# Performance work log

Measured on AMD Instinct MI355X. Metric: run time of the kernel, lower is better.

The kernel has to match this reference:

```python
import jax, jax.numpy as jnp
import numpy as np

EMBED = 1024
HEADS = 16
HEAD_DIM = EMBED // HEADS


def setup_inputs() -> dict:
    key = jax.random.key(0)
    ks = jax.random.split(key, 5)
    s = 0.02
    x = jax.random.normal(ks[0], (2, 2048, EMBED), dtype=jnp.float32)
    W_qkv = jax.random.normal(ks[1], (EMBED, 3 * EMBED), dtype=jnp.float32) * s
    b_qkv = jnp.zeros((3 * EMBED,), dtype=jnp.float32)
    W_proj = jax.random.normal(ks[2], (EMBED, EMBED), dtype=jnp.float32) * s
    b_proj = jnp.zeros((EMBED,), dtype=jnp.float32)
    return {"x": x, "W_qkv": W_qkv, "b_qkv": b_qkv, "W_proj": W_proj, "b_proj": b_proj}


def reference(x, W_qkv, b_qkv, W_proj, b_proj):
    B, N, _ = x.shape
    scale = HEAD_DIM ** -0.5
    qkv = x @ W_qkv + b_qkv                     # [B,N,3E]
    qkv = qkv.reshape(B, N, 3, HEADS, HEAD_DIM)
    q = qkv[:, :, 0].transpose(0, 2, 1, 3) * scale  # [B,H,N,D]
    k = qkv[:, :, 1].transpose(0, 2, 1, 3)
    v = qkv[:, :, 2].transpose(0, 2, 1, 3)
    attn = jnp.einsum('bhnd,bhmd->bhnm', q, k)  # [B,H,N,N]
    attn = jax.nn.softmax(attn, axis=-1)
    out = jnp.einsum('bhnm,bhmd->bhnd', attn, v)  # [B,H,N,D]
    out = out.transpose(0, 2, 1, 3).reshape(B, N, HEADS * HEAD_DIM)
    return out @ W_proj + b_proj
```

## Files before the change

### kernel.cpp

```cpp
#include <hip/hip_runtime.h>
#include <hip/hip_bf16.h>
#include <stdint.h>

typedef unsigned short u16;
typedef __bf16 bf16x8 __attribute__((ext_vector_type(8)));
typedef float f32x4 __attribute__((ext_vector_type(4)));

__device__ __forceinline__ u16 f2bf(float f) {
    union { float f; unsigned u; } x; x.f = f;
    unsigned u = x.u;
    u += 0x7FFFu + ((u >> 16) & 1u);
    return (u16)(u >> 16);
}

typedef __attribute__((address_space(1))) void gvoid;
typedef __attribute__((address_space(3))) void lvoid;
__device__ __forceinline__ void gl2lds16(const void* g, void* l) {
    __builtin_amdgcn_global_load_lds((gvoid*)g, (lvoid*)l, 16, 0, 0);
}

__global__ __launch_bounds__(256) void prep_kernel(
    const float* __restrict__ x, u16* __restrict__ xb,
    const float* __restrict__ Wqkv, u16* __restrict__ wqkvT,
    const float* __restrict__ Wproj, u16* __restrict__ wprojT)
{
    __shared__ u16 tile[64][65];
    const int blk = blockIdx.x;
    const int tid = threadIdx.x;

    if (blk < 2048) {
        const size_t i = ((size_t)blk * 256 + tid) * 8;
        float4 a = *(const float4*)(x + i);
        float4 b = *(const float4*)(x + i + 4);
        ushort4 oa, ob;
        oa.x = f2bf(a.x); oa.y = f2bf(a.y); oa.z = f2bf(a.z); oa.w = f2bf(a.w);
        ob.x = f2bf(b.x); ob.y = f2bf(b.y); ob.z = f2bf(b.z); ob.w = f2bf(b.w);
        *(ushort4*)(xb + i) = oa;
        *(ushort4*)(xb + i + 4) = ob;
        return;
    }
    const float* in; u16* out; int rows, cols, bx, by;
    if (blk < 2816) { int t = blk - 2048; in = Wqkv;  out = wqkvT;  rows = 1024; cols = 3072; bx = t % 48; by = t / 48; }
    else            { int t = blk - 2816; in = Wproj; out = wprojT; rows = 1024; cols = 1024; bx = t % 16; by = t / 16; }
#pragma unroll
    for (int i = 0; i < 16; i++) {
        int e = i * 256 + tid;
        int r = e >> 6, c = e & 63;
        tile[r][c] = f2bf(in[(size_t)(by * 64 + r) * cols + bx * 64 + c]);
    }
    __syncthreads();
#pragma unroll
    for (int i = 0; i < 16; i++) {
        int e = i * 256 + tid;
        int r = e >> 6, c = e & 63;
        out[(size_t)(bx * 64 + r) * rows + by * 64 + c] = tile[c][r];
    }
}

__global__ __launch_bounds__(256) void transpose_v(
    const u16* __restrict__ in, u16* __restrict__ out)
{
    __shared__ u16 tile[64][65];
    const int bh = blockIdx.y;
    const int t0 = blockIdx.x * 64;
    const u16* ip = in + ((size_t)bh * 2048 + t0) * 64;
    u16* op = out + (size_t)bh * 64 * 2048 + t0;
    const int tid = threadIdx.x;
#pragma unroll
    for (int i = 0; i < 16; i++) {
        int e = i * 256 + tid;
        int r = e >> 6, c = e & 63;
        tile[r][c] = ip[(size_t)r * 64 + c];
    }
    __syncthreads();
#pragma unroll
    for (int i = 0; i < 16; i++) {
        int e = i * 256 + tid;
        int d = e >> 6, tt = e & 63;
        op[(size_t)d * 2048 + tt] = tile[tt][d];
    }
}

__global__ __launch_bounds__(256) void gemm_qkv(
    const u16* __restrict__ A, const u16* __restrict__ Bt,
    const float* __restrict__ bias,
    u16* __restrict__ q, u16* __restrict__ ko, u16* __restrict__ vo)
{
    constexpr int K = 1024;
    __shared__ __align__(16) u16 sA[128 * 64];
    __shared__ __align__(16) u16 sB[128 * 64];
    const int tid = threadIdx.x;
    const int wave = tid >> 6, lane = tid & 63;
    const int quad = lane >> 4, l16 = lane & 15;
    const int wm = (wave >> 1) * 64, wn = (wave & 1) * 64;
    const int m0 = blockIdx.y * 128, n0 = blockIdx.x * 128;
    const int srow = lane >> 3;
    const int scol = (lane & 7) * 8;

    f32x4 acc[4][4];
#pragma unroll
    for (int i = 0; i < 4; i++)
#pragma unroll
        for (int j = 0; j < 4; j++)
#pragma unroll
            for (int r = 0; r < 4; r++) acc[i][j][r] = 0.f;

    for (int kt = 0; kt < K; kt += 64) {
        __syncthreads();
#pragma unroll
        for (int t = 0; t < 4; t++) {
            int rb = wave * 32 + t * 8;
            gl2lds16(A  + (size_t)(m0 + rb + srow) * K + kt + scol, &sA[rb * 64]);
            gl2lds16(Bt + (size_t)(n0 + rb + srow) * K + kt + scol, &sB[rb * 64]);
        }
        __syncthreads();
#pragma unroll
        for (int kk = 0; kk < 64; kk += 32) {
            bf16x8 af[4], bfr[4];
#pragma unroll
            for (int t = 0; t < 4; t++) {
                af[t]  = *(const bf16x8*)&sA[(wm + t * 16 + l16) * 64 + kk + quad * 8];
                bfr[t] = *(const bf16x8*)&sB[(wn + t * 16 + l16) * 64 + kk + quad * 8];
            }
#pragma unroll
            for (int i = 0; i < 4; i++)
#pragma unroll
                for (int j = 0; j < 4; j++)
                    acc[i][j] = __builtin_amdgcn_mfma_f32_16x16x32_bf16(
                        af[i], bfr[j], acc[i][j], 0, 0, 0);
        }
    }

    const float QSCALE = 0.18033688011112042f;
#pragma unroll
    for (int i = 0; i < 4; i++) {
#pragma unroll
        for (int j = 0; j < 4; j++) {
            int n = n0 + wn + j * 16 + l16;
            float bv = bias[n];
            int which = n >> 10, rem = n & 1023;
            int h = rem >> 6, d = rem & 63;
#pragma unroll
            for (int r = 0; r < 4; r++) {
                int m = m0 + wm + i * 16 + quad * 4 + r;
                float v = acc[i][j][r] + bv;
                int b = m >> 11, t = m & 2047;
                size_t idx = ((size_t)(b * 16 + h) * 2048 + t) * 64 + d;
                if (which == 0)
                    q[idx] = f2bf(v * QSCALE);
                else if (which == 1)
                    ko[idx] = f2bf(v);
                else
                    vo[idx] = f2bf(v);
            }
        }
    }
}

__global__ __launch_bounds__(256) void attn_kernel(
    const u16* __restrict__ q, const u16* __restrict__ ko,
    const u16* __restrict__ vt, u16* __restrict__ o)
{
    __shared__ __align__(16) u16 sQ[128 * 72];
    __shared__ __align__(16) u16 sK[64 * 72];
    __shared__ __align__(16) u16 sV[80 * 72];
    __shared__ __align__(16) float sPf[128 * 68];

    const int tid = threadIdx.x;
    const int wave = tid >> 6, lane = tid & 63;
    const int quad = lane >> 4, l16 = lane & 15;

    const int lid = blockIdx.x;
    const int xcd = lid & 7, idx = lid >> 3;
    const int h = xcd * 2 + (idx & 1);
    const int b = (idx >> 1) & 1;
    const int q0 = (idx >> 2) * 128;
    const size_t bh = (size_t)(b * 16 + h);

    const u16* qp  = q  + bh * 2048 * 64;
    const u16* kp  = ko + bh * 2048 * 64;
    const u16* vtp = vt + bh * 64 * 2048;

    const int sr0 = tid >> 3;
    const int sc0 = (tid & 7) * 8;
    const int sr1 = (tid + 256) >> 3;
    const int sc1 = sc0;

#pragma unroll
    for (int i = 0; i < 4; i++) {
        int c = tid + i * 256;
        int r = c >> 3, cc = c & 7;
        *(uint4*)&sQ[r * 72 + cc * 8] =
            *(const uint4*)(qp + (size_t)(q0 + r) * 64 + cc * 8);
    }
#pragma unroll
    for (int i = 0; i < 4; i++) {
        int c = tid + i * 256;
        sV[(64 + (c >> 6)) * 72 + (c & 63)] = 0x3F80;
    }

    uint4 pk0 = *(const uint4*)(kp + (size_t)sr0 * 64 + sc0);
    uint4 pk1 = *(const uint4*)(kp + (size_t)sr1 * 64 + sc1);
    uint4 pv0 = *(const uint4*)(vtp + (size_t)sr0 * 2048 + sc0);
    uint4 pv1 = *(const uint4*)(vtp + (size_t)sr1 * 2048 + sc1);

    __syncthreads();

    bf16x8 qf[2][2];
#pragma unroll
    for (int i = 0; i < 2; i++)
#pragma unroll
        for (int k2 = 0; k2 < 2; k2++)
            qf[i][k2] = *(const bf16x8*)&sQ[(wave * 32 + i * 16 + l16) * 72 + k2 * 32 + quad * 8];

    f32x4 accO[2][4];
    f32x4 accL[2];
#pragma unroll
    for (int i = 0; i < 2; i++) {
#pragma unroll
        for (int r = 0; r < 4; r++) accL[i][r] = 0.f;
#pragma unroll
        for (int j = 0; j < 4; j++)
#pragma unroll
            for (int r = 0; r < 4; r++) accO[i][j][r] = 0.f;
    }

    for (int kt = 0; kt < 2048; kt += 64) {
        __syncthreads();
        *(uint4*)&sK[sr0 * 72 + sc0] = pk0;
        *(uint4*)&sK[sr1 * 72 + sc1] = pk1;
        *(uint4*)&sV[sr0 * 72 + sc0] = pv0;
        *(uint4*)&sV[sr1 * 72 + sc1] = pv1;
        if (kt + 64 < 2048) {
            int nt = kt + 64;
            pk0 = *(const uint4*)(kp + (size_t)(nt + sr0) * 64 + sc0);
            pk1 = *(const uint4*)(kp + (size_t)(nt + sr1) * 64 + sc1);
            pv0 = *(const uint4*)(vtp + (size_t)sr0 * 2048 + nt + sc0);
            pv1 = *(const uint4*)(vtp + (size_t)sr1 * 2048 + nt + sc1);
        }
        __syncthreads();

        f32x4 S[2][4];
#pragma unroll
        for (int i = 0; i < 2; i++)
#pragma unroll
            for (int j = 0; j < 4; j++)
#pragma unroll
                for (int r = 0; r < 4; r++) S[i][j][r] = 0.f;
#pragma unroll
        for (int k2 = 0; k2 < 2; k2++) {
            int kk = k2 * 32;
#pragma unroll
            for (int j = 0; j < 4; j++) {
                bf16x8 bk = *(const bf16x8*)&sK[(j * 16 + l16) * 72 + kk + quad * 8];
                S[0][j] = __builtin_amdgcn_mfma_f32_16x16x32_bf16(qf[0][k2], bk, S[0][j], 0, 0, 0);
                S[1][j] = __builtin_amdgcn_mfma_f32_16x16x32_bf16(qf[1][k2], bk, S[1][j], 0, 0, 0);
            }
        }

        float* pw = &sPf[(wave * 32 + quad * 4) * 68 + l16];
#pragma unroll
        for (int i = 0; i < 2; i++)
#pragma unroll
            for (int j = 0; j < 4; j++)
#pragma unroll
                for (int r = 0; r < 4; r++)
                    pw[(i * 16 + r) * 68 + j * 16] = __builtin_amdgcn_exp2f(S[i][j][r]);

#pragma unroll
        for (int k2 = 0; k2 < 2; k2++) {
            int kk = k2 * 32;
            bf16x8 bv[5];
#pragma unroll
            for (int j = 0; j < 5; j++)
                bv[j] = *(const bf16x8*)&sV[(j * 16 + l16) * 72 + kk + quad * 8];
#pragma unroll
            for (int i = 0; i < 2; i++) {
                const uint32_t* pr =
                    (const uint32_t*)&sPf[(wave * 32 + i * 16 + l16) * 68 + kk + quad * 8];
                uint4 w0 = *(const uint4*)pr;
                uint4 w1 = *(const uint4*)(pr + 4);
                union { uint32_t u[4]; bf16x8 v; } ap;
                ap.u[0] = __builtin_amdgcn_perm(w0.y, w0.x, 0x07060302u);
                ap.u[1] = __builtin_amdgcn_perm(w0.w, w0.z, 0x07060302u);
                ap.u[2] = __builtin_amdgcn_perm(w1.y, w1.x, 0x07060302u);
                ap.u[3] = __builtin_amdgcn_perm(w1.w, w1.z, 0x07060302u);
#pragma unroll
                for (int j = 0; j < 4; j++)
                    accO[i][j] = __builtin_amdgcn_mfma_f32_16x16x32_bf16(ap.v, bv[j], accO[i][j], 0, 0, 0);
                accL[i] = __builtin_amdgcn_mfma_f32_16x16x32_bf16(ap.v, bv[4], accL[i], 0, 0, 0);
            }
        }
    }

#pragma unroll
    for (int i = 0; i < 2; i++)
#pragma unroll
        for (int r = 0; r < 4; r++) {
            float inv = 1.f / accL[i][r];
            size_t row = (size_t)b * 2048 + q0 + wave * 32 + i * 16 + quad * 4 + r;
#pragma unroll
            for (int j = 0; j < 4; j++)
                o[row * 1024 + h * 64 + j * 16 + l16] = f2bf(accO[i][j][r] * inv);
        }
}

__global__ __launch_bounds__(256) void gemm_proj(
    const u16* __restrict__ A, const u16* __restrict__ Bt,
    const float* __restrict__ bias, float* __restrict__ out)
{
    constexpr int K = 1024;
    __shared__ __align__(16) u16 sA[128 * 64];
    __shared__ __align__(16) u16 sB[128 * 64];
    const int tid = threadIdx.x;
    const int wave = tid >> 6, lane = tid & 63;
    const int quad = lane >> 4, l16 = lane & 15;
    const int wm = (wave >> 1) * 64, wn = (wave & 1) * 64;
    const int m0 = blockIdx.y * 128, n0 = blockIdx.x * 128;
    const int srow = lane >> 3;
    const int scol = (lane & 7) * 8;

    f32x4 acc[4][4];
#pragma unroll
    for (int i = 0; i < 4; i++)
#pragma unroll
        for (int j = 0; j < 4; j++)
#pragma unroll
            for (int r = 0; r < 4; r++) acc[i][j][r] = 0.f;

    for (int kt = 0; kt < K; kt += 64) {
        __syncthreads();
#pragma unroll
        for (int t = 0; t < 4; t++) {
            int rb = wave * 32 + t * 8;
            gl2lds16(A  + (size_t)(m0 + rb + srow) * K + kt + scol, &sA[rb * 64]);
            gl2lds16(Bt + (size_t)(n0 + rb + srow) * K + kt + scol, &sB[rb * 64]);
        }
        __syncthreads();
#pragma unroll
        for (int kk = 0; kk < 64; kk += 32) {
            bf16x8 af[4], bfr[4];
#pragma unroll
            for (int t = 0; t < 4; t++) {
                af[t]  = *(const bf16x8*)&sA[(wm + t * 16 + l16) * 64 + kk + quad * 8];
                bfr[t] = *(const bf16x8*)&sB[(wn + t * 16 + l16) * 64 + kk + quad * 8];
            }
#pragma unroll
            for (int i = 0; i < 4; i++)
#pragma unroll
                for (int j = 0; j < 4; j++)
                    acc[i][j] = __builtin_amdgcn_mfma_f32_16x16x32_bf16(
                        af[i], bfr[j], acc[i][j], 0, 0, 0);
        }
    }

#pragma unroll
    for (int i = 0; i < 4; i++) {
#pragma unroll
        for (int j = 0; j < 4; j++) {
            int n = n0 + wn + j * 16 + l16;
            float bv = bias[n];
#pragma unroll
            for (int r = 0; r < 4; r++) {
                int m = m0 + wm + i * 16 + quad * 4 + r;
                out[(size_t)m * 1024 + n] = acc[i][j][r] + bv;
            }
        }
    }
}

extern "C" void kernel_launch(void* const* d_in, const int* in_sizes, int n_in,
                              void* d_out, int out_size, void* d_ws, size_t ws_size,
                              hipStream_t stream) {
    const float* x     = (const float*)d_in[0];
    const float* Wqkv  = (const float*)d_in[1];
    const float* bqkv  = (const float*)d_in[2];
    const float* Wproj = (const float*)d_in[3];
    const float* bproj = (const float*)d_in[4];
    float* out = (float*)d_out;
    char* ws = (char*)d_ws;

    u16* wqkvT  = (u16*)(ws);
    u16* wprojT = (u16*)(ws +  6291456);
    u16* xb     = (u16*)(ws +  8388608);
    u16* qb     = (u16*)(ws + 16777216);
    u16* kb     = (u16*)(ws + 25165824);
    u16* vtb    = (u16*)(ws + 33554432);
    u16* ob     = (u16*)(ws + 41943040);
    u16* vb     = ob;

    prep_kernel<<<dim3(3072), 256, 0, stream>>>(x, xb, Wqkv, wqkvT, Wproj, wprojT);
    gemm_qkv<<<dim3(24, 32), 256, 0, stream>>>(xb, wqkvT, bqkv, qb, kb, vb);
    transpose_v<<<dim3(32, 32), 256, 0, stream>>>(vb, vtb);
    attn_kernel<<<dim3(512), 256, 0, stream>>>(qb, kb, vtb, ob);
    gemm_proj<<<dim3(8, 32), 256, 0, stream>>>(ob, wprojT, bproj, out);
}
```

Before: 222.4 us.

## Stage QKV epilogue through LDS for vector stores; store P as bf16

The QKV GEMM epilogue now writes scaled, biased bf16 results into a padded shared tile and then emits coalesced 16-byte stores into the per-head q/k/v layouts, replacing scattered 2-byte stores. In the attention kernel, probabilities are stored in shared memory directly as bf16 (truncated) rather than fp32 followed by a perm-based repack, which halves LDS traffic and footprint. The row-sum MFMA now uses a register constant of ones instead of extra rows in sV. Truncation instead of rounding of P slightly changes numerics, and the epilogue gains an extra barrier and an LDS round trip.

```diff
diff --git a/kernel.cpp b/kernel.cpp
--- a/kernel.cpp
+++ b/kernel.cpp
@@ -87,8 +87,9 @@
     u16* __restrict__ q, u16* __restrict__ ko, u16* __restrict__ vo)
 {
     constexpr int K = 1024;
-    __shared__ __align__(16) u16 sA[128 * 64];
-    __shared__ __align__(16) u16 sB[128 * 64];
+    __shared__ __align__(16) u16 smem[128 * 132];
+    u16* sA = smem;
+    u16* sB = smem + 8192;
     const int tid = threadIdx.x;
     const int wave = tid >> 6, lane = tid & 63;
     const int quad = lane >> 4, l16 = lane & 15;
@@ -132,28 +133,36 @@
     }
 
     const float QSCALE = 0.18033688011112042f;
+    __syncthreads();
 #pragma unroll
     for (int i = 0; i < 4; i++) {
 #pragma unroll
         for (int j = 0; j < 4; j++) {
             int n = n0 + wn + j * 16 + l16;
             float bv = bias[n];
-            int which = n >> 10, rem = n & 1023;
-            int h = rem >> 6, d = rem & 63;
+            float sc = (n < 1024) ? QSCALE : 1.0f;
 #pragma unroll
             for (int r = 0; r < 4; r++) {
-                int m = m0 + wm + i * 16 + quad * 4 + r;
-                float v = acc[i][j][r] + bv;
-                int b = m >> 11, t = m & 2047;
-                size_t idx = ((size_t)(b * 16 + h) * 2048 + t) * 64 + d;
-                if (which == 0)
-                    q[idx] = f2bf(v * QSCALE);
-                else if (which == 1)
-                    ko[idx] = f2bf(v);
-                else
-                    vo[idx] = f2bf(v);
-            }
-        }
+                float v = (acc[i][j][r] + bv) * sc;
+                smem[(wm + i * 16 + quad * 4 + r) * 132 + wn + j * 16 + l16] = f2bf(v);
+            }
+        }
+    }
+    __syncthreads();
+
+#pragma unroll
+    for (int it = 0; it < 8; it++) {
+        int c = it * 256 + tid;
+        int m_l = c >> 4;
+        int n8 = (c & 15) * 8;
+        uint4 w = *(const uint4*)&smem[m_l * 132 + n8];
+        int n = n0 + n8;
+        int which = n >> 10, rem = n & 1023;
+        int h = rem >> 6, d = rem & 63;
+        int m = m0 + m_l;
+        int b = m >> 11, t = m & 2047;
+        u16* dst = (which == 0) ? q : (which == 1) ? ko : vo;
+        *(uint4*)(dst + ((size_t)(b * 16 + h) * 2048 + t) * 64 + d) = w;
     }
 }
 
@@ -163,8 +172,8 @@
 {
     __shared__ __align__(16) u16 sQ[128 * 72];
     __shared__ __align__(16) u16 sK[64 * 72];
-    __shared__ __align__(16) u16 sV[80 * 72];
-    __shared__ __align__(16) float sPf[128 * 68];
+    __shared__ __align__(16) u16 sV[64 * 72];
+    __shared__ __align__(16) u16 sP[128 * 72];
 
     const int tid = threadIdx.x;
     const int wave = tid >> 6, lane = tid & 63;
@@ -184,7 +193,6 @@
     const int sr0 = tid >> 3;
     const int sc0 = (tid & 7) * 8;
     const int sr1 = (tid + 256) >> 3;
-    const int sc1 = sc0;
 
 #pragma unroll
     for (int i = 0; i < 4; i++) {
@@ -193,16 +201,14 @@
         *(uint4*)&sQ[r * 72 + cc * 8] =
             *(const uint4*)(qp + (size_t)(q0 + r) * 64 + cc * 8);
     }
-#pragma unroll
-    for (int i = 0; i < 4; i++) {
-        int c = tid + i * 256;
-        sV[(64 + (c >> 6)) * 72 + (c & 63)] = 0x3F80;
-    }
+
+    union { uint32_t u[4]; bf16x8 v; } ones;
+    ones.u[0] = ones.u[1] = ones.u[2] = ones.u[3] = 0x3F803F80u;
 
     uint4 pk0 = *(const uint4*)(kp + (size_t)sr0 * 64 + sc0);
-    uint4 pk1 = *(const uint4*)(kp + (size_t)sr1 * 64 + sc1);
+    uint4 pk1 = *(const uint4*)(kp + (size_t)sr1 * 64 + sc0);
     uint4 pv0 = *(const uint4*)(vtp + (size_t)sr0 * 2048 + sc0);
-    uint4 pv1 = *(const uint4*)(vtp + (size_t)sr1 * 2048 + sc1);
+    uint4 pv1 = *(const uint4*)(vtp + (size_t)sr1 * 2048 + sc0);
 
     __syncthreads();
 
@@ -228,15 +234,15 @@
     for (int kt = 0; kt < 2048; kt += 64) {
         __syncthreads();
         *(uint4*)&sK[sr0 * 72 + sc0] = pk0;
-        *(uint4*)&sK[sr1 * 72 + sc1] = pk1;
+        *(uint4*)&sK[sr1 * 72 + sc0] = pk1;
         *(uint4*)&sV[sr0 * 72 + sc0] = pv0;
-        *(uint4*)&sV[sr1 * 72 + sc1] = pv1;
+        *(uint4*)&sV[sr1 * 72 + sc0] = pv1;
         if (kt + 64 < 2048) {
             int nt = kt + 64;
             pk0 = *(const uint4*)(kp + (size_t)(nt + sr0) * 64 + sc0);
-            pk1 = *(const uint4*)(kp + (size_t)(nt + sr1) * 64 + sc1);
+            pk1 = *(const uint4*)(kp + (size_t)(nt + sr1) * 64 + sc0);
             pv0 = *(const uint4*)(vtp + (size_t)sr0 * 2048 + nt + sc0);
-            pv1 = *(const uint4*)(vtp + (size_t)sr1 * 2048 + nt + sc1);
+            pv1 = *(const uint4*)(vtp + (size_t)sr1 * 2048 + nt + sc0);
         }
         __syncthreads();
 
@@ -258,37 +264,32 @@
             }
         }
 
-        float* pw = &sPf[(wave * 32 + quad * 4) * 68 + l16];
+        u16* pw = &sP[(wave * 32 + quad * 4) * 72 + l16];
 #pragma unroll
         for (int i = 0; i < 2; i++)
 #pragma unroll
             for (int j = 0; j < 4; j++)
 #pragma unroll
-                for (int r = 0; r < 4; r++)
-                    pw[(i * 16 + r) * 68 + j * 16] = __builtin_amdgcn_exp2f(S[i][j][r]);
+                for (int r = 0; r < 4; r++) {
+                    union { float f; uint32_t u; } e;
+                    e.f = __builtin_amdgcn_exp2f(S[i][j][r]);
+                    pw[(i * 16 + r) * 72 + j * 16] = (u16)(e.u >> 16);
+                }
 
 #pragma unroll
         for (int k2 = 0; k2 < 2; k2++) {
             int kk = k2 * 32;
-            bf16x8 bv[5];
-#pragma unroll
-            for (int j = 0; j < 5; j++)
+            bf16x8 bv[4];
+#pragma unroll
+            for (int j = 0; j < 4; j++)
                 bv[j] = *(const bf16x8*)&sV[(j * 16 + l16) * 72 + kk + quad * 8];
 #pragma unroll
             for (int i = 0; i < 2; i++) {
-                const uint32_t* pr =
-                    (const uint32_t*)&sPf[(wave * 32 + i * 16 + l16) * 68 + kk + quad * 8];
-                uint4 w0 = *(const uint4*)pr;
-                uint4 w1 = *(const uint4*)(pr + 4);
-                union { uint32_t u[4]; bf16x8 v; } ap;
-                ap.u[0] = __builtin_amdgcn_perm(w0.y, w0.x, 0x07060302u);
-                ap.u[1] = __builtin_amdgcn_perm(w0.w, w0.z, 0x07060302u);
-                ap.u[2] = __builtin_amdgcn_perm(w1.y, w1.x, 0x07060302u);
-                ap.u[3] = __builtin_amdgcn_perm(w1.w, w1.z, 0x07060302u);
+                bf16x8 ap = *(const bf16x8*)&sP[(wave * 32 + i * 16 + l16) * 72 + kk + quad * 8];
 #pragma unroll
                 for (int j = 0; j < 4; j++)
-                    accO[i][j] = __builtin_amdgcn_mfma_f32_16x16x32_bf16(ap.v, bv[j], accO[i][j], 0, 0, 0);
-                accL[i] = __builtin_amdgcn_mfma_f32_16x16x32_bf16(ap.v, bv[4], accL[i], 0, 0, 0);
+                    accO[i][j] = __builtin_amdgcn_mfma_f32_16x16x32_bf16(ap, bv[j], accO[i][j], 0, 0, 0);
+                accL[i] = __builtin_amdgcn_mfma_f32_16x16x32_bf16(ap, ones.v, accL[i], 0, 0, 0);
             }
         }
     }
```

Result: no change. 218.5 us (-1.8%).
